# Kernel optimization log

Hardware: AMD Instinct MI355X
Metric: run time of the kernel (lower is better)

The kernel has to match this reference:

```python
import jax, jax.numpy as jnp
import numpy as np

N = 4608      # total nodes (48 graphs x 96 nodes)
B = 48
NPG = 96
D = 512       # vec_dim
XD = 16       # x_dim
E = N * 32    # GAT edges
L = 6         # GAT layers


def _w(k, shape, fan_in):
    return jax.random.normal(k, shape, jnp.float32) * (1.0 / np.sqrt(fan_in))


def setup_inputs() -> dict:
    key = jax.random.key(0)
    ks = jax.random.split(key, 24)
    x = jax.random.normal(ks[0], (N, XD), jnp.float32)
    xyz = jax.random.normal(ks[1], (N, 3), jnp.float32)
    edge_index = jax.random.randint(ks[2], (2, E), 0, N, dtype=jnp.int32)
    ptr = (jnp.arange(B + 1) * NPG).astype(jnp.int32)
    # complete graph with replacement per segment (torch.combinations order: i<=j)
    i, j = np.triu_indices(NPG)
    offs = (np.arange(B) * NPG)[:, None]
    cloud_edge_index = jnp.asarray(
        np.stack([(i[None, :] + offs).reshape(-1), (j[None, :] + offs).reshape(-1)]),
        jnp.int32)
    return {
        'x': x, 'edge_index': edge_index, 'ptr': ptr, 'xyz': xyz,
        'cloud_edge_index': cloud_edge_index,
        'x_proj_w': _w(ks[3], (XD, D), XD), 'x_proj_b': jnp.zeros((D,), jnp.float32),
        'gat_wl': _w(ks[4], (L, D, D), D), 'gat_bl': jnp.zeros((L, D), jnp.float32),
        'gat_wr': _w(ks[5], (L, D, D), D), 'gat_br': jnp.zeros((L, D), jnp.float32),
        'gat_att': _w(ks[6], (L, D), D), 'gat_bias': jnp.zeros((L, D), jnp.float32),
        'gat_ln_g': jnp.ones((L - 1, D), jnp.float32), 'gat_ln_b': jnp.zeros((L - 1, D), jnp.float32),
        'cg_xyz_w': _w(ks[7], (3, D), 3),
        'cg_bn_g': jnp.ones((D,), jnp.float32), 'cg_bn_b': jnp.zeros((D,), jnp.float32),
        'cg_lin1_w': _w(ks[8], (D, D), D), 'cg_lin1_b': jnp.zeros((D,), jnp.float32),
        'cg_ln_g': jnp.ones((D,), jnp.float32), 'cg_ln_b': jnp.zeros((D,), jnp.float32),
        'lin_w': _w(ks[9], (D, D), D), 'lin_b': jnp.zeros((D,), jnp.float32),
        'bn_g': jnp.ones((D,), jnp.float32), 'bn_b': jnp.zeros((D,), jnp.float32),
    }


def _batchnorm(t, g, b):
    mu = t.mean(0)
    v = ((t - mu) ** 2).mean(0)
    return (t - mu) / jnp.sqrt(v + 1e-5) * g + b


def _forward(x, edge_index, cloud_edge_index, x_proj_w, x_proj_b, gat_wl, gat_bl,
             gat_wr, gat_br, gat_att, gat_bias, gat_ln_g, gat_ln_b, cg_xyz_w,
             cg_bn_g, cg_bn_b, cg_lin1_w, cg_lin1_b, cg_ln_g, cg_ln_b,
             lin_w, lin_b, bn_g, bn_b, xyz):
    n = x.shape[0]
    h = x @ x_proj_w + x_proj_b  # [N, D]
    # ---- GATv2 stack (heads=1, self-loops added, eval mode: no dropout) ----
    loops = jnp.arange(n, dtype=edge_index.dtype)
    ei = jnp.concatenate([edge_index, jnp.stack([loops, loops])], axis=1)
    src, dst = ei[0], ei[1]
    xg = h
    for l in range(L):
        xl = xg @ gat_wl[l] + gat_bl[l]
        xr = xg @ gat_wr[l] + gat_br[l]
        e = jax.nn.leaky_relu(xl[src] + xr[dst], 0.2) @ gat_att[l]  # [E+N]
        m = jax.ops.segment_max(e, dst, num_segments=n)
        ew = jnp.exp(e - m[dst])
        den = jax.ops.segment_sum(ew, dst, num_segments=n)
        alpha = ew / den[dst]
        out = jax.ops.segment_sum(alpha[:, None] * xl[src], dst, num_segments=n) + gat_bias[l]
        if l < L - 1:
            # PyG LayerNorm, mode='graph', batch=None: normalize over all elements
            mu = out.mean()
            sd = jnp.sqrt(((out - mu) ** 2).mean())
            out = (out - mu) / (sd + 1e-5) * gat_ln_g[l] + gat_ln_b[l]
            out = jax.nn.relu(out)
        xg = out
    # ---- CloudGraph (complete graph gather-compute-scatter) ----
    a, b = cloud_edge_index[0], cloud_edge_index[1]
    rx = h[a] - h[b]          # [Ec, D]
    rz = xyz[a] - xyz[b]      # [Ec, 3]
    sq = (rz ** 2).sum(-1)
    dist = jnp.where(sq > 0, jnp.sqrt(jnp.where(sq > 0, sq, 1.0)), 0.0)
    w = jnp.exp(-dist)[:, None]
    p1 = jax.ops.segment_sum(jax.nn.relu((w * rx) @ cg_lin1_w + cg_lin1_b), a, num_segments=n)
    mu1 = p1.mean(-1, keepdims=True)
    v1 = ((p1 - mu1) ** 2).mean(-1, keepdims=True)
    ln1 = (p1 - mu1) / jnp.sqrt(v1 + 1e-5) * cg_ln_g + cg_ln_b
    p2 = jax.ops.segment_sum(jax.nn.relu(rz @ cg_xyz_w), a, num_segments=n)
    xc = h + ln1 + _batchnorm(p2, cg_bn_g, cg_bn_b)
    # ---- fuse + final norm ----
    return _batchnorm((h + xg + xc) @ lin_w + lin_b, bn_g, bn_b)


def reference(x, edge_index, ptr, xyz, cloud_edge_index, x_proj_w, x_proj_b,
              gat_wl, gat_bl, gat_wr, gat_br, gat_att, gat_bias, gat_ln_g,
              gat_ln_b, cg_xyz_w, cg_bn_g, cg_bn_b, cg_lin1_w, cg_lin1_b,
              cg_ln_g, cg_ln_b, lin_w, lin_b, bn_g, bn_b):
    return _forward(x, edge_index, cloud_edge_index, x_proj_w, x_proj_b, gat_wl,
                    gat_bl, gat_wr, gat_br, gat_att, gat_bias, gat_ln_g,
                    gat_ln_b, cg_xyz_w, cg_bn_g, cg_bn_b, cg_lin1_w, cg_lin1_b,
                    cg_ln_g, cg_ln_b, lin_w, lin_b, bn_g, bn_b, xyz)
```

## Files before the change

### kernel.cpp

```cpp
#include <hip/hip_runtime.h>
#include <hip/hip_bf16.h>

#define NN 4608
#define BG 48
#define NPG 96
#define DD 512
#define XDIM 16
#define EREAL 147456
#define NLAYER 6
#define NK 262144
#define TRIU 4656

typedef __hip_bfloat16 bf16;
typedef short short8 __attribute__((ext_vector_type(8)));
typedef float f32x4 __attribute__((ext_vector_type(4)));
typedef float f32x2 __attribute__((ext_vector_type(2)));

__device__ __forceinline__ float s2f(short s) {
  return __uint_as_float(((unsigned int)(unsigned short)s) << 16);
}
__device__ __forceinline__ short f2bs(float f) {
  bf16 h = __float2bfloat16(f);
  short s;
  __builtin_memcpy(&s, &h, 2);
  return s;
}
__device__ __forceinline__ unsigned char f2f8(float v) {
  return (unsigned char)(__builtin_amdgcn_cvt_pk_fp8_f32(v, v, 0, false) & 0xff);
}
__device__ __forceinline__ void f8x4(unsigned int w, float* o) {
  f32x2 a = __builtin_amdgcn_cvt_pk_f32_fp8(w, false);
  f32x2 b = __builtin_amdgcn_cvt_pk_f32_fp8(w, true);
  o[0] = a[0]; o[1] = a[1]; o[2] = b[0]; o[3] = b[1];
}

typedef const __attribute__((address_space(1))) unsigned int ga_u32;
typedef __attribute__((address_space(3))) unsigned int ls_u32;
__device__ __forceinline__ void gl16(const void* g, void* l) {
  __builtin_amdgcn_global_load_lds((ga_u32*)g, (ls_u32*)l, 16, 0, 0);
}

__global__ __launch_bounds__(256) void k_wt(const float* __restrict__ wl,
                                            const float* __restrict__ wr,
                                            const float* __restrict__ cg,
                                            const float* __restrict__ lin,
                                            bf16* __restrict__ Wt,
                                            int* __restrict__ counts,
                                            float* __restrict__ statsAll) {
  if (blockIdx.z == 0) {
    int id = (blockIdx.y * 16 + blockIdx.x) * 256 + threadIdx.x;
    if (id < NN) counts[id] = 0;
    if (id < 5 * 32) statsAll[id] = 0.f;
  }
  __shared__ float tile[32][33];
  int z = blockIdx.z;
  const float* src = (z < 6) ? wl + (size_t)z * NK
                   : (z < 12) ? wr + (size_t)(z - 6) * NK
                   : (z == 12) ? cg : lin;
  bf16* dst = Wt + (size_t)z * NK;
  int c = threadIdx.x & 31;
  int r0 = threadIdx.x >> 5;
  int bx = blockIdx.x * 32, by = blockIdx.y * 32;
#pragma unroll
  for (int i = 0; i < 4; i++) {
    int r = r0 + i * 8;
    tile[r][c] = src[(size_t)(by + r) * 512 + bx + c];
  }
  __syncthreads();
#pragma unroll
  for (int i = 0; i < 4; i++) {
    int r = r0 + i * 8;
    dst[(size_t)(bx + r) * 512 + by + c] = __float2bfloat16(tile[c][r]);
  }
}

__global__ void k_xproj(const float* __restrict__ x, const float* __restrict__ w,
                        const float* __restrict__ b, const int* __restrict__ ei,
                        const float* __restrict__ xyz,
                        bf16* __restrict__ h_bf, int* __restrict__ counts,
                        float* __restrict__ ep) {
  int i = blockIdx.x * blockDim.x + threadIdx.x;
  if (i >= NN * DD) return;
  if (i < EREAL) atomicAdd(&counts[ei[EREAL + i]], 1);
  if (i < NN * NPG) {
    int n = i / NPG, e = i - n * NPG;
    int p = n % NPG;
    if (e < NPG - p) {
      int g = n / NPG;
      int slot = g * TRIU + p * NPG - (p * (p - 1)) / 2 + e;
      int j = n + e;
      float dx = xyz[n * 3] - xyz[j * 3];
      float dy = xyz[n * 3 + 1] - xyz[j * 3 + 1];
      float dz = xyz[n * 3 + 2] - xyz[j * 3 + 2];
      float sq = dx * dx + dy * dy + dz * dz;
      float dist = (sq > 0.f) ? sqrtf(sq) : 0.f;
      float4 v;
      v.x = dx; v.y = dy; v.z = dz; v.w = __expf(-dist);
      *(float4*)&ep[(size_t)slot * 4] = v;
    }
  }
  int n = i >> 9, d = i & 511;
  float acc = b[d];
#pragma unroll
  for (int k = 0; k < XDIM; k++) acc += x[n * XDIM + k] * w[k * DD + d];
  h_bf[i] = __float2bfloat16(acc);
}

__global__ void k_scan(const int* __restrict__ counts, int* offsets, int* cursor) {
  __shared__ int part[256];
  __shared__ int pre[256];
  int t = threadIdx.x;
  int base = t * 18;
  int s = 0;
#pragma unroll
  for (int i = 0; i < 18; i++) s += counts[base + i];
  part[t] = s;
  __syncthreads();
  if (t == 0) {
    int r = 0;
    for (int i = 0; i < 256; i++) { pre[i] = r; r += part[i]; }
  }
  __syncthreads();
  int run = pre[t];
#pragma unroll
  for (int i = 0; i < 18; i++) {
    offsets[base + i] = run;
    cursor[base + i] = run;
    run += counts[base + i];
  }
  if (t == 0) offsets[NN] = EREAL;
}
__global__ void k_scatter(const int* __restrict__ ei, int* cursor, int* ssrc) {
  int e = blockIdx.x * blockDim.x + threadIdx.x;
  if (e < EREAL) {
    int s = ei[e], d = ei[EREAL + e];
    int pos = atomicAdd(&cursor[d], 1);
    ssrc[pos] = s;
  }
}

__global__ __launch_bounds__(256) void k_ln(const bf16* __restrict__ in,
                                            bf16* __restrict__ out,
                                            const float* __restrict__ stats,
                                            const float* __restrict__ g,
                                            const float* __restrict__ b) {
  float s = 0.f, ss = 0.f;
#pragma unroll
  for (int i = 0; i < 16; i++) { s += stats[i]; ss += stats[16 + i]; }
  const float invM = 1.f / ((float)NN * (float)DD);
  float mu = s * invM;
  float var = ss * invM - mu * mu;
  float sd = sqrtf(fmaxf(var, 0.f));
  float inv = 1.f / (sd + 1e-5f);
  int i = blockIdx.x * 256 + threadIdx.x;
  int base = i * 8;
  int d0 = base & 511;
  short8 raw = *(const short8*)&in[base];
  short8 pk;
#pragma unroll
  for (int k = 0; k < 8; k++) {
    float t = fmaxf((s2f(raw[k]) - mu) * inv * g[d0 + k] + b[d0 + k], 0.f);
    pk[k] = f2bs(t);
  }
  *(short8*)&out[base] = pk;
}

__global__ __launch_bounds__(256) void k_gemm(
    const bf16* __restrict__ Abf,
    const bf16* __restrict__ B0, const bf16* __restrict__ B1,
    const float* __restrict__ bias0, const float* __restrict__ bias1,
    float* __restrict__ C0, float* __restrict__ C1,
    bf16* __restrict__ Cb0, bf16* __restrict__ Cb1,
    unsigned char* __restrict__ Cf8_0, unsigned char* __restrict__ Cf8_1,
    float* __restrict__ zptr, int zn,
    float* __restrict__ csum, float* __restrict__ csq, int nzl) {
  if (zptr && blockIdx.x == 0) {
    for (int i = threadIdx.x; i < zn; i += 256) zptr[i] = 0.f;
  }
  __shared__ __align__(16) bf16 As[2][128 * 32];
  __shared__ __align__(16) bf16 Bs[2][64 * 32];
  __shared__ float cs[64], cq[64];
  int cpx = gridDim.x >> 3;
  int wgid = (blockIdx.x & 7) * cpx + (blockIdx.x >> 3);
  int mi = wgid >> nzl;
  int r = wgid & ((1 << nzl) - 1);
  int z = r >> 3;
  int m0 = mi * 128, n0 = (r & 7) * 64;

  const bf16* B = z ? B1 : B0;
  const float* bias = z ? bias1 : bias0;
  float* C = z ? C1 : C0;
  bf16* Cb = z ? Cb1 : Cb0;
  unsigned char* Cf8 = z ? Cf8_1 : Cf8_0;
  int tid = threadIdx.x;
  int lane = tid & 63, wid = tid >> 6;
  int mh = (wid >> 1) * 64, nh = (wid & 1) * 32;
  int l15 = lane & 15, quad = lane >> 4;
  int lrow = lane >> 2, lkc = (lane & 3) * 8;

  if (csum && tid < 64) { cs[tid] = 0.f; cq[tid] = 0.f; }

  const bf16* aSrc0 = Abf + (size_t)(m0 + wid * 16 + lrow) * 512 + lkc;
  const bf16* aSrc1 = Abf + (size_t)(m0 + 64 + wid * 16 + lrow) * 512 + lkc;
  const bf16* bSrc  = B   + (size_t)(n0 + wid * 16 + lrow) * 512 + lkc;

#define STAGE(bi, kk) do {                                  \
    gl16(aSrc0 + (kk) * 32, &As[bi][wid * 512]);            \
    gl16(aSrc1 + (kk) * 32, &As[bi][2048 + wid * 512]);     \
    gl16(bSrc  + (kk) * 32, &Bs[bi][wid * 512]);            \
  } while (0)

  f32x4 acc[4][2];
#pragma unroll
  for (int mt = 0; mt < 4; mt++)
#pragma unroll
    for (int nt = 0; nt < 2; nt++) acc[mt][nt] = (f32x4)0.f;

  STAGE(0, 0);
  __syncthreads();

#pragma unroll
  for (int kt = 0; kt < 16; kt++) {
    const int cur = kt & 1;
    if (kt < 15) STAGE(cur ^ 1, kt + 1);
    short8 af[4], bfr[2];
#pragma unroll
    for (int mt = 0; mt < 4; mt++)
      af[mt] = *(const short8*)&As[cur][(mh + mt * 16 + l15) * 32 + quad * 8];
#pragma unroll
    for (int nt = 0; nt < 2; nt++)
      bfr[nt] = *(const short8*)&Bs[cur][(nh + nt * 16 + l15) * 32 + quad * 8];
#pragma unroll
    for (int mt = 0; mt < 4; mt++)
#pragma unroll
      for (int nt = 0; nt < 2; nt++)
        acc[mt][nt] = __builtin_amdgcn_mfma_f32_16x16x32_bf16(
            af[mt], bfr[nt], acc[mt][nt], 0, 0, 0);
    __syncthreads();
  }
#undef STAGE

  float colS[2] = {0.f, 0.f}, colQ[2] = {0.f, 0.f};
#pragma unroll
  for (int mt = 0; mt < 4; mt++) {
#pragma unroll
    for (int nt = 0; nt < 2; nt++) {
      int col = n0 + nh + nt * 16 + l15;
      float bv = bias ? bias[col] : 0.f;
#pragma unroll
      for (int r2 = 0; r2 < 4; r2++) {
        int row = m0 + mh + mt * 16 + quad * 4 + r2;
        float v = acc[mt][nt][r2] + bv;
        if (C) C[(size_t)row * 512 + col] = v;
        if (Cb) Cb[(size_t)row * 512 + col] = __float2bfloat16(v);
        if (Cf8) Cf8[(size_t)row * 512 + col] = f2f8(v);
        if (csum) { colS[nt] += v; colQ[nt] += v * v; }
      }
    }
  }
  if (csum) {
#pragma unroll
    for (int nt = 0; nt < 2; nt++) {
      atomicAdd(&cs[nh + nt * 16 + l15], colS[nt]);
      atomicAdd(&cq[nh + nt * 16 + l15], colQ[nt]);
    }
    __syncthreads();
    if (tid < 64) {
      atomicAdd(&csum[n0 + tid], cs[tid]);
      atomicAdd(&csq[n0 + tid], cq[tid]);
    }
  }
}

__global__ __launch_bounds__(256) void k_gat_edge(const unsigned char* __restrict__ xl8,
                                                  const bf16* __restrict__ xr,
                                                  const float* __restrict__ att,
                                                  const float* __restrict__ bias,
                                                  const int* __restrict__ offs,
                                                  const int* __restrict__ ssrc,
                                                  bf16* __restrict__ out,
                                                  float* __restrict__ statsOut) {
  __shared__ float redS[4], redSS[4];
  int wave = (blockIdx.x * blockDim.x + threadIdx.x) >> 6;
  int lane = threadIdx.x & 63;
  int wid = threadIdx.x >> 6;
  if (wave < NN) {
    int n = wave;
    int base = lane * 8;
    float xrv[8], attv[8], acc[8];
    short8 xr8 = *(const short8*)&xr[(size_t)n * 512 + base];
#pragma unroll
    for (int k = 0; k < 8; k++) {
      xrv[k] = s2f(xr8[k]);
      attv[k] = att[base + k];
    }
    float m0, lsum;
    {
      uint2 q = *(const uint2*)&xl8[(size_t)n * 512 + base];
      float xs[8];
      f8x4(q.x, xs);
      f8x4(q.y, xs + 4);
      float sc0 = 0.f;
#pragma unroll
      for (int k = 0; k < 8; k++) {
        acc[k] = xs[k];
        float t = xs[k] + xrv[k];
        t = (t > 0.f) ? t : 0.2f * t;
        sc0 += attv[k] * t;
      }
#pragma unroll
      for (int off = 32; off >= 1; off >>= 1) sc0 += __shfl_xor(sc0, off, 64);
      m0 = sc0;
      lsum = 1.f;
    }
    int e0 = offs[n], e1 = offs[n + 1];
    int e = e0;
    for (; e + 3 < e1; e += 4) {
      int s0 = ssrc[e], s1 = ssrc[e + 1], s2 = ssrc[e + 2], s3 = ssrc[e + 3];
      uint2 q0 = *(const uint2*)&xl8[(size_t)s0 * 512 + base];
      uint2 q1 = *(const uint2*)&xl8[(size_t)s1 * 512 + base];
      uint2 q2 = *(const uint2*)&xl8[(size_t)s2 * 512 + base];
      uint2 q3 = *(const uint2*)&xl8[(size_t)s3 * 512 + base];
      float x0[8], x1[8], x2[8], x3[8];
      f8x4(q0.x, x0); f8x4(q0.y, x0 + 4);
      f8x4(q1.x, x1); f8x4(q1.y, x1 + 4);
      f8x4(q2.x, x2); f8x4(q2.y, x2 + 4);
      f8x4(q3.x, x3); f8x4(q3.y, x3 + 4);
      float c0 = 0.f, c1 = 0.f, c2 = 0.f, c3 = 0.f;
#pragma unroll
      for (int k = 0; k < 8; k++) {
        float t0 = x0[k] + xrv[k]; t0 = (t0 > 0.f) ? t0 : 0.2f * t0; c0 += attv[k] * t0;
        float t1 = x1[k] + xrv[k]; t1 = (t1 > 0.f) ? t1 : 0.2f * t1; c1 += attv[k] * t1;
        float t2 = x2[k] + xrv[k]; t2 = (t2 > 0.f) ? t2 : 0.2f * t2; c2 += attv[k] * t2;
        float t3 = x3[k] + xrv[k]; t3 = (t3 > 0.f) ? t3 : 0.2f * t3; c3 += attv[k] * t3;
      }
#pragma unroll
      for (int off = 32; off >= 1; off >>= 1) {
        c0 += __shfl_xor(c0, off, 64);
        c1 += __shfl_xor(c1, off, 64);
        c2 += __shfl_xor(c2, off, 64);
        c3 += __shfl_xor(c3, off, 64);
      }
      float p0 = __expf(c0 - m0), p1 = __expf(c1 - m0);
      float p2 = __expf(c2 - m0), p3 = __expf(c3 - m0);
      lsum += p0 + p1 + p2 + p3;
#pragma unroll
      for (int k = 0; k < 8; k++)
        acc[k] += p0 * x0[k] + p1 * x1[k] + p2 * x2[k] + p3 * x3[k];
    }
    for (; e < e1; ++e) {
      int s0 = ssrc[e];
      uint2 q = *(const uint2*)&xl8[(size_t)s0 * 512 + base];
      float x0[8];
      f8x4(q.x, x0);
      f8x4(q.y, x0 + 4);
      float sc0 = 0.f;
#pragma unroll
      for (int k = 0; k < 8; k++) {
        float t0 = x0[k] + xrv[k];
        t0 = (t0 > 0.f) ? t0 : 0.2f * t0;
        sc0 += attv[k] * t0;
      }
#pragma unroll
      for (int off = 32; off >= 1; off >>= 1) sc0 += __shfl_xor(sc0, off, 64);
      float p0 = __expf(sc0 - m0);
      lsum += p0;
#pragma unroll
      for (int k = 0; k < 8; k++) acc[k] += p0 * x0[k];
    }
    float inv = 1.f / lsum;
    float o[8];
    float s = 0.f, ss = 0.f;
    short8 o8;
#pragma unroll
    for (int k = 0; k < 8; k++) {
      o[k] = acc[k] * inv + bias[base + k];
      s += o[k];
      ss += o[k] * o[k];
      o8[k] = f2bs(o[k]);
    }
    *(short8*)&out[(size_t)n * 512 + base] = o8;
    if (statsOut) {
#pragma unroll
      for (int off = 32; off >= 1; off >>= 1) {
        s += __shfl_xor(s, off, 64);
        ss += __shfl_xor(ss, off, 64);
      }
      if (lane == 0) { redS[wid] = s; redSS[wid] = ss; }
    }
  }
  if (statsOut) {
    __syncthreads();
    if (threadIdx.x == 0) {
      float a = redS[0] + redS[1] + redS[2] + redS[3];
      float b = redSS[0] + redSS[1] + redSS[2] + redSS[3];
      int slot = blockIdx.x & 15;
      atomicAdd(&statsOut[slot], a);
      atomicAdd(&statsOut[16 + slot], b);
    }
  }
}

__global__ __launch_bounds__(256) void k_cloud(const bf16* __restrict__ g1,
                                               const float* __restrict__ ep,
                                               const float* __restrict__ lin1b,
                                               const float* __restrict__ w3,
                                               float* __restrict__ p1,
                                               float* __restrict__ p2) {
  int w = (blockIdx.x * blockDim.x + threadIdx.x) >> 6;
  int lane = threadIdx.x & 63;
  if (w >= NN * 2) return;
  int qf = w & 3;
  int pi = w >> 2;
  int g = pi / 48, pp = pi % 48;
  int d0 = qf * 128 + lane * 2;
  float bb0 = lin1b[d0], bb1 = lin1b[d0 + 1];
  float w00 = w3[d0], w01 = w3[d0 + 1];
  float w10 = w3[512 + d0], w11 = w3[512 + d0 + 1];
  float w20 = w3[1024 + d0], w21 = w3[1024 + d0 + 1];

#pragma unroll
  for (int half = 0; half < 2; half++) {
    int p = half ? (NPG - 1 - pp) : pp;
    int n = g * NPG + p;
    int cnt = NPG - p;
    int slot0 = g * TRIU + p * NPG - (p * (p - 1)) / 2;
    const bf16* grow = &g1[(size_t)n * 512 + d0];
    unsigned int giw = *(const unsigned int*)grow;
    float gi0 = s2f((short)(giw & 0xffff));
    float gi1 = s2f((short)(giw >> 16));
    float a10 = 0.f, a11 = 0.f, a20 = 0.f, a21 = 0.f;
    float b10 = 0.f, b11 = 0.f, b20 = 0.f, b21 = 0.f;
    int e = 0;
    for (; e + 3 < cnt; e += 4) {
      int sb = __builtin_amdgcn_readfirstlane(slot0 + e);
      float4 pa = *(const float4*)&ep[(size_t)sb * 4];
      float4 pb = *(const float4*)&ep[(size_t)(sb + 1) * 4];
      float4 pc = *(const float4*)&ep[(size_t)(sb + 2) * 4];
      float4 pd = *(const float4*)&ep[(size_t)(sb + 3) * 4];
      unsigned int ga = *(const unsigned int*)&grow[(size_t)e * 512];
      unsigned int gb = *(const unsigned int*)&grow[(size_t)(e + 1) * 512];
      unsigned int gc = *(const unsigned int*)&grow[(size_t)(e + 2) * 512];
      unsigned int gd = *(const unsigned int*)&grow[(size_t)(e + 3) * 512];
      float t;
      t = fmaf(pa.w, gi0 - s2f((short)(ga & 0xffff)), bb0); a10 += fmaxf(t, 0.f);
      t = fmaf(pa.w, gi1 - s2f((short)(ga >> 16)), bb1);    a11 += fmaxf(t, 0.f);
      t = fmaf(pb.w, gi0 - s2f((short)(gb & 0xffff)), bb0); b10 += fmaxf(t, 0.f);
      t = fmaf(pb.w, gi1 - s2f((short)(gb >> 16)), bb1);    b11 += fmaxf(t, 0.f);
      t = fmaf(pc.w, gi0 - s2f((short)(gc & 0xffff)), bb0); a10 += fmaxf(t, 0.f);
      t = fmaf(pc.w, gi1 - s2f((short)(gc >> 16)), bb1);    a11 += fmaxf(t, 0.f);
      t = fmaf(pd.w, gi0 - s2f((short)(gd & 0xffff)), bb0); b10 += fmaxf(t, 0.f);
      t = fmaf(pd.w, gi1 - s2f((short)(gd >> 16)), bb1);    b11 += fmaxf(t, 0.f);
      t = pa.x * w00 + pa.y * w10 + pa.z * w20; a20 += fmaxf(t, 0.f);
      t = pa.x * w01 + pa.y * w11 + pa.z * w21; a21 += fmaxf(t, 0.f);
      t = pb.x * w00 + pb.y * w10 + pb.z * w20; b20 += fmaxf(t, 0.f);
      t = pb.x * w01 + pb.y * w11 + pb.z * w21; b21 += fmaxf(t, 0.f);
      t = pc.x * w00 + pc.y * w10 + pc.z * w20; a20 += fmaxf(t, 0.f);
      t = pc.x * w01 + pc.y * w11 + pc.z * w21; a21 += fmaxf(t, 0.f);
      t = pd.x * w00 + pd.y * w10 + pd.z * w20; b20 += fmaxf(t, 0.f);
      t = pd.x * w01 + pd.y * w11 + pd.z * w21; b21 += fmaxf(t, 0.f);
    }
    for (; e < cnt; ++e) {
      float4 pa = *(const float4*)&ep[(size_t)(slot0 + e) * 4];
      unsigned int ga = *(const unsigned int*)&grow[(size_t)e * 512];
      float t;
      t = fmaf(pa.w, gi0 - s2f((short)(ga & 0xffff)), bb0); a10 += fmaxf(t, 0.f);
      t = fmaf(pa.w, gi1 - s2f((short)(ga >> 16)), bb1);    a11 += fmaxf(t, 0.f);
      t = pa.x * w00 + pa.y * w10 + pa.z * w20; a20 += fmaxf(t, 0.f);
      t = pa.x * w01 + pa.y * w11 + pa.z * w21; a21 += fmaxf(t, 0.f);
    }
    float2 o1, o2;
    o1.x = a10 + b10; o1.y = a11 + b11;
    o2.x = a20 + b20; o2.y = a21 + b21;
    *(float2*)&p1[(size_t)n * 512 + d0] = o1;
    *(float2*)&p2[(size_t)n * 512 + d0] = o2;
  }
}

__global__ __launch_bounds__(256) void k_cloud_epi(
    const float* __restrict__ p1, const float* __restrict__ p2,
    const bf16* __restrict__ h_bf, const bf16* __restrict__ xg_bf,
    const float* __restrict__ colsum, const float* __restrict__ colsq,
    const float* __restrict__ lng, const float* __restrict__ lnb,
    const float* __restrict__ bng, const float* __restrict__ bnb,
    bf16* __restrict__ s_bf, float* __restrict__ zptr) {
  if (blockIdx.x == 0) {
    for (int i = threadIdx.x; i < 1024; i += 256) zptr[i] = 0.f;
  }
  int wave = (blockIdx.x * blockDim.x + threadIdx.x) >> 6;
  int lane = threadIdx.x & 63;
  if (wave >= NN) return;
  int n = wave;
  size_t rb = (size_t)n * 512 + lane * 8;
  int base = lane * 8;
  float v[8];
  float s = 0.f;
#pragma unroll
  for (int k = 0; k < 8; k++) {
    v[k] = p1[rb + k];
    s += v[k];
  }
#pragma unroll
  for (int off = 32; off >= 1; off >>= 1) s += __shfl_xor(s, off, 64);
  float mu = s * (1.f / 512.f);
  float ss = 0.f;
#pragma unroll
  for (int k = 0; k < 8; k++) {
    float t = v[k] - mu;
    ss += t * t;
  }
#pragma unroll
  for (int off = 32; off >= 1; off >>= 1) ss += __shfl_xor(ss, off, 64);
  float inv = 1.f / sqrtf(ss * (1.f / 512.f) + 1e-5f);
  short8 hb = *(const short8*)&h_bf[rb];
  short8 xb = *(const short8*)&xg_bf[rb];
  short8 o8;
#pragma unroll
  for (int k = 0; k < 8; k++) {
    int d = base + k;
    float ln1 = (v[k] - mu) * inv * lng[d] + lnb[d];
    float cmu = colsum[d] * (1.f / NN);
    float cvar = colsq[d] * (1.f / NN) - cmu * cmu;
    float cinv = 1.f / sqrtf(fmaxf(cvar, 0.f) + 1e-5f);
    float bnv = (p2[rb + k] - cmu) * cinv * bng[d] + bnb[d];
    float out = 2.f * s2f(hb[k]) + s2f(xb[k]) + ln1 + bnv;
    o8[k] = f2bs(out);
  }
  *(short8*)&s_bf[rb] = o8;
}

__global__ void k_col_reduce(const float* __restrict__ x, float* colsum, float* colsq) {
  int r0 = blockIdx.x * 128;
  int c0 = threadIdx.x;
  float s0 = 0.f, q0 = 0.f, s1 = 0.f, q1 = 0.f;
  for (int r = r0; r < r0 + 128; ++r) {
    float v = x[(size_t)r * 512 + c0];
    s0 += v;
    q0 += v * v;
    float w = x[(size_t)r * 512 + c0 + 256];
    s1 += w;
    q1 += w * w;
  }
  atomicAdd(&colsum[c0], s0);
  atomicAdd(&colsq[c0], q0);
  atomicAdd(&colsum[c0 + 256], s1);
  atomicAdd(&colsq[c0 + 256], q1);
}
__global__ void k_bn_out(const float* __restrict__ y, const float* __restrict__ colsum,
                         const float* __restrict__ colsq, const float* __restrict__ g,
                         const float* __restrict__ b, float* __restrict__ out) {
  int i = blockIdx.x * blockDim.x + threadIdx.x;
  if (i >= NN * DD) return;
  int d = i & 511;
  float mu = colsum[d] * (1.f / NN);
  float var = colsq[d] * (1.f / NN) - mu * mu;
  float inv = 1.f / sqrtf(fmaxf(var, 0.f) + 1e-5f);
  out[i] = (y[i] - mu) * inv * g[d] + b[d];
}

extern "C" void kernel_launch(void* const* d_in, const int* in_sizes, int n_in,
                              void* d_out, int out_size, void* d_ws, size_t ws_size,
                              hipStream_t stream) {
  const float* x = (const float*)d_in[0];
  const int* ei = (const int*)d_in[1];
  const float* xyz = (const float*)d_in[3];
  const float* x_proj_w = (const float*)d_in[5];
  const float* x_proj_b = (const float*)d_in[6];
  const float* gat_wl = (const float*)d_in[7];
  const float* gat_bl = (const float*)d_in[8];
  const float* gat_wr = (const float*)d_in[9];
  const float* gat_br = (const float*)d_in[10];
  const float* gat_att = (const float*)d_in[11];
  const float* gat_bias = (const float*)d_in[12];
  const float* gat_ln_g = (const float*)d_in[13];
  const float* gat_ln_b = (const float*)d_in[14];
  const float* cg_xyz_w = (const float*)d_in[15];
  const float* cg_bn_g = (const float*)d_in[16];
  const float* cg_bn_b = (const float*)d_in[17];
  const float* cg_lin1_w = (const float*)d_in[18];
  const float* cg_lin1_b = (const float*)d_in[19];
  const float* cg_ln_g = (const float*)d_in[20];
  const float* cg_ln_b = (const float*)d_in[21];
  const float* lin_w = (const float*)d_in[22];
  const float* lin_b = (const float*)d_in[23];
  const float* bn_g = (const float*)d_in[24];
  const float* bn_b = (const float*)d_in[25];

  const size_t ND = (size_t)NN * DD;
  char* w = (char*)d_ws;
  float* p1 = (float*)w;       w += ND * 4;
  float* p2 = (float*)w;       w += ND * 4;
  bf16* h_bf = (bf16*)w;       w += ND * 2;
  bf16* xg_bf = (bf16*)w;      w += ND * 2;
  bf16* g1_bf = (bf16*)w;      w += ND * 2;
  bf16* xr_bf = (bf16*)w;      w += ND * 2;
  unsigned char* xl_f8 = (unsigned char*)w; w += ND;
  bf16* Wt = (bf16*)w;         w += (size_t)14 * NK * 2;
  float* eparam = (float*)w;   w += (size_t)BG * TRIU * 16;
  int* counts = (int*)w;       w += NN * 4;
  int* offs = (int*)w;         w += (NN + 4) * 4;
  int* cursor = (int*)w;       w += NN * 4;
  int* ssrc = (int*)w;         w += EREAL * 4;
  float* statsAll = (float*)w; w += 5 * 32 * 4;
  float* colsum = (float*)w;   w += 512 * 4;
  float* colsq = (float*)w;    w += 512 * 4;
  float* colsum2 = (float*)w;  w += 512 * 4;
  float* colsq2 = (float*)w;   w += 512 * 4;
  float* y = p1;
  bf16* s_bf = h_bf;
  bf16* aln_bf = g1_bf;

  const int TPB = 256;
  const int ND_BLK = (int)((ND + TPB - 1) / TPB);

  k_wt<<<dim3(16, 16, 14), TPB, 0, stream>>>(gat_wl, gat_wr, cg_lin1_w, lin_w, Wt,
                                             counts, statsAll);
  k_xproj<<<ND_BLK, TPB, 0, stream>>>(x, x_proj_w, x_proj_b, ei, xyz, h_bf,
                                      counts, eparam);
  k_scan<<<1, 256, 0, stream>>>(counts, offs, cursor);
  k_scatter<<<(EREAL + TPB - 1) / TPB, TPB, 0, stream>>>(ei, cursor, ssrc);

  for (int l = 0; l < NLAYER; l++) {
    const bf16* A;
    if (l == 0) {
      A = h_bf;
    } else {
      k_ln<<<(int)(ND / 8 / TPB), TPB, 0, stream>>>(
          xg_bf, aln_bf, statsAll + 32 * (l - 1),
          gat_ln_g + (size_t)(l - 1) * DD, gat_ln_b + (size_t)(l - 1) * DD);
      A = aln_bf;
    }
    k_gemm<<<576, TPB, 0, stream>>>(
        A, Wt + (size_t)l * NK, Wt + (size_t)(6 + l) * NK,
        gat_bl + l * DD, gat_br + l * DD, nullptr, nullptr, nullptr, xr_bf,
        xl_f8, nullptr, nullptr, 0, nullptr, nullptr, 4);
    float* sOut = (l < NLAYER - 1) ? statsAll + 32 * l : nullptr;
    k_gat_edge<<<NN / 4, TPB, 0, stream>>>(xl_f8, xr_bf, gat_att + l * DD,
                                           gat_bias + l * DD, offs, ssrc,
                                           xg_bf, sOut);
  }

  k_gemm<<<288, TPB, 0, stream>>>(
      h_bf, Wt + (size_t)12 * NK, Wt + (size_t)12 * NK, nullptr, nullptr,
      nullptr, nullptr, g1_bf, g1_bf, nullptr, nullptr,
      colsum, 1024, nullptr, nullptr, 3);
  k_cloud<<<NN / 2, TPB, 0, stream>>>(g1_bf, eparam, cg_lin1_b, cg_xyz_w, p1, p2);
  k_col_reduce<<<36, 256, 0, stream>>>(p2, colsum, colsq);
  k_cloud_epi<<<NN / 4, TPB, 0, stream>>>(p1, p2, h_bf, xg_bf, colsum, colsq,
                                          cg_ln_g, cg_ln_b, cg_bn_g, cg_bn_b,
                                          s_bf, colsum2);

  k_gemm<<<288, TPB, 0, stream>>>(
      s_bf, Wt + (size_t)13 * NK, Wt + (size_t)13 * NK, lin_b, lin_b,
      y, y, nullptr, nullptr, nullptr, nullptr,
      nullptr, 0, colsum2, colsq2, 3);
  k_bn_out<<<ND_BLK, TPB, 0, stream>>>(y, colsum2, colsq2, bn_g, bn_b,
                                       (float*)d_out);
}
```

Before: 557.5 us.

## Double GEMM K-tile to 64 with XOR-swizzled LDS layout

The bf16 MFMA GEMM now stages K-tiles of 64 instead of 32, halving the number of loop iterations and __syncthreads barriers. The LDS tiles use an XOR swizzle on 16-byte chunks by row so the wider rows avoid bank conflicts on fragment reads. This doubles shared memory per block, which may lower occupancy, and raises fragment register use.

```diff
diff --git a/kernel.cpp b/kernel.cpp
--- a/kernel.cpp
+++ b/kernel.cpp
@@ -177,8 +177,8 @@
   if (zptr && blockIdx.x == 0) {
     for (int i = threadIdx.x; i < zn; i += 256) zptr[i] = 0.f;
   }
-  __shared__ __align__(16) bf16 As[2][128 * 32];
-  __shared__ __align__(16) bf16 Bs[2][64 * 32];
+  __shared__ __align__(16) bf16 As[2][128 * 64];
+  __shared__ __align__(16) bf16 Bs[2][64 * 64];
   __shared__ float cs[64], cq[64];
   int cpx = gridDim.x >> 3;
   int wgid = (blockIdx.x & 7) * cpx + (blockIdx.x >> 3);
@@ -196,18 +196,23 @@
   int lane = tid & 63, wid = tid >> 6;
   int mh = (wid >> 1) * 64, nh = (wid & 1) * 32;
   int l15 = lane & 15, quad = lane >> 4;
-  int lrow = lane >> 2, lkc = (lane & 3) * 8;
+  int lr8 = lane >> 3;
+  int ls8 = lane & 7;
+  int c16l = ls8 ^ (lr8 & 7);
+  int swzr = (l15 & 7) * 8;
 
   if (csum && tid < 64) { cs[tid] = 0.f; cq[tid] = 0.f; }
 
-  const bf16* aSrc0 = Abf + (size_t)(m0 + wid * 16 + lrow) * 512 + lkc;
-  const bf16* aSrc1 = Abf + (size_t)(m0 + 64 + wid * 16 + lrow) * 512 + lkc;
-  const bf16* bSrc  = B   + (size_t)(n0 + wid * 16 + lrow) * 512 + lkc;
-
-#define STAGE(bi, kk) do {                                  \
-    gl16(aSrc0 + (kk) * 32, &As[bi][wid * 512]);            \
-    gl16(aSrc1 + (kk) * 32, &As[bi][2048 + wid * 512]);     \
-    gl16(bSrc  + (kk) * 32, &Bs[bi][wid * 512]);            \
+  const bf16* aSrc = Abf + (size_t)(m0 + wid * 32 + lr8) * 512 + c16l * 8;
+  const bf16* bSrc = B   + (size_t)(n0 + wid * 16 + lr8) * 512 + c16l * 8;
+
+#define STAGE(bi, kt) do {                                              \
+    gl16(aSrc + (kt) * 64,            &As[bi][(wid * 32     ) * 64]);   \
+    gl16(aSrc + (kt) * 64 +  8 * 512, &As[bi][(wid * 32 +  8) * 64]);   \
+    gl16(aSrc + (kt) * 64 + 16 * 512, &As[bi][(wid * 32 + 16) * 64]);   \
+    gl16(aSrc + (kt) * 64 + 24 * 512, &As[bi][(wid * 32 + 24) * 64]);   \
+    gl16(bSrc + (kt) * 64,            &Bs[bi][(wid * 16     ) * 64]);   \
+    gl16(bSrc + (kt) * 64 +  8 * 512, &Bs[bi][(wid * 16 +  8) * 64]);   \
   } while (0)
 
   f32x4 acc[4][2];
@@ -220,22 +225,29 @@
   __syncthreads();
 
 #pragma unroll
-  for (int kt = 0; kt < 16; kt++) {
+  for (int kt = 0; kt < 8; kt++) {
     const int cur = kt & 1;
-    if (kt < 15) STAGE(cur ^ 1, kt + 1);
-    short8 af[4], bfr[2];
-#pragma unroll
-    for (int mt = 0; mt < 4; mt++)
-      af[mt] = *(const short8*)&As[cur][(mh + mt * 16 + l15) * 32 + quad * 8];
-#pragma unroll
-    for (int nt = 0; nt < 2; nt++)
-      bfr[nt] = *(const short8*)&Bs[cur][(nh + nt * 16 + l15) * 32 + quad * 8];
-#pragma unroll
-    for (int mt = 0; mt < 4; mt++)
+    if (kt < 7) STAGE(cur ^ 1, kt + 1);
+    short8 af[2][4], bfr[2][2];
+#pragma unroll
+    for (int kk = 0; kk < 2; kk++) {
+#pragma unroll
+      for (int mt = 0; mt < 4; mt++)
+        af[kk][mt] = *(const short8*)&As[cur][(mh + mt * 16 + l15) * 64 +
+                                             (((kk * 4 + quad) * 8) ^ swzr)];
 #pragma unroll
       for (int nt = 0; nt < 2; nt++)
-        acc[mt][nt] = __builtin_amdgcn_mfma_f32_16x16x32_bf16(
-            af[mt], bfr[nt], acc[mt][nt], 0, 0, 0);
+        bfr[kk][nt] = *(const short8*)&Bs[cur][(nh + nt * 16 + l15) * 64 +
+                                              (((kk * 4 + quad) * 8) ^ swzr)];
+    }
+#pragma unroll
+    for (int kk = 0; kk < 2; kk++)
+#pragma unroll
+      for (int mt = 0; mt < 4; mt++)
+#pragma unroll
+        for (int nt = 0; nt < 2; nt++)
+          acc[mt][nt] = __builtin_amdgcn_mfma_f32_16x16x32_bf16(
+              af[kk][mt], bfr[kk][nt], acc[mt][nt], 0, 0, 0);
     __syncthreads();
   }
 #undef STAGE
```

Result: faster. 541.5 us (-2.9%).
